# Kernel tuning notes

Hardware: AMD Instinct MI355X
Metric: run time of the kernel (lower is better)

## Reference

```python
import jax, jax.numpy as jnp
import numpy as np
from jax import lax

EPS = 1e-5
QUANT_BITS = 16  # Conv2dShift default input fixed-point bits


def round_fixed(x, quant_bits=QUANT_BITS):
    # fixed-point rounding of activations with straight-through estimator
    scale = 2.0 ** (quant_bits - 1)
    xq = jnp.round(x * scale) / scale
    return x + lax.stop_gradient(xq - x)


def shift_conv3x3(x, w_shift, stride=1):
    # w_shift already holds sign * 2^shift power-of-two weights (see setup)
    x = round_fixed(x)
    return lax.conv_general_dilated(
        x, w_shift, window_strides=(stride, stride), padding=[(1, 1), (1, 1)],
        dimension_numbers=("NCHW", "OIHW", "NCHW"))


def adder_conv3x3(x, w):
    # AdderNet: out[n,co,h,w] = -sum_{ci,kh,kw} |patch - w[co,ci,kh,kw]|
    Co = w.shape[0]
    # patches: [N, C*3*3, H, W], feature ordering (c, kh, kw) matches w.reshape
    p = lax.conv_general_dilated_patches(
        x, filter_shape=(3, 3), window_strides=(1, 1), padding=[(1, 1), (1, 1)])
    wf = w.reshape(Co, -1)

    def per_out_channel(wc):  # wc: [C*9]
        return -jnp.sum(jnp.abs(p - wc[None, :, None, None]), axis=1)  # [N,H,W]

    out = lax.map(per_out_channel, wf)  # [Co, N, H, W] (sequential: bounds memory)
    return jnp.transpose(out, (1, 0, 2, 3))


def batch_norm(x, gamma, beta):
    # training-mode BN (batch statistics), matching nn.BatchNorm2d default forward
    m = jnp.mean(x, axis=(0, 2, 3), keepdims=True)
    v = jnp.var(x, axis=(0, 2, 3), keepdims=True)
    xn = (x - m) * lax.rsqrt(v + EPS)
    return xn * gamma.reshape(1, -1, 1, 1) + beta.reshape(1, -1, 1, 1)


def _quantize_shift_weights(w, weight_bits=5):
    # DeepShift PS: weight -> sign * 2^round(log2|w|), shift clipped
    sign = jnp.where(w >= 0, 1.0, -1.0)
    shift = jnp.round(jnp.log2(jnp.abs(w) + 1e-12))
    shift = jnp.clip(shift, -(2.0 ** (weight_bits - 1) - 1.0), 0.0)
    return sign * jnp.exp2(shift)


def setup_inputs() -> dict:
    key = jax.random.key(0)
    ks = jax.random.split(key, 9)
    N, C, H, W = 64, 128, 32, 32
    planes = 128
    fan = 1.0 / np.sqrt(C * 9)
    x = jax.random.normal(ks[0], (N, C, H, W), dtype=jnp.float32)
    w_shift1 = _quantize_shift_weights(
        jax.random.normal(ks[1], (planes, C, 3, 3), dtype=jnp.float32) * fan)
    w_add1 = jax.random.normal(ks[2], (planes, planes, 3, 3), dtype=jnp.float32) * fan
    w_shift2 = _quantize_shift_weights(
        jax.random.normal(ks[3], (planes, planes, 3, 3), dtype=jnp.float32) * fan)
    w_add2 = jax.random.normal(ks[4], (planes, planes, 3, 3), dtype=jnp.float32) * fan
    gamma1 = jnp.ones((planes,), jnp.float32)
    beta1 = jnp.zeros((planes,), jnp.float32)
    gamma2 = jnp.ones((planes,), jnp.float32)
    beta2 = jnp.zeros((planes,), jnp.float32)
    return {"x": x, "w_shift1": w_shift1, "w_add1": w_add1, "gamma1": gamma1,
            "beta1": beta1, "w_shift2": w_shift2, "w_add2": w_add2,
            "gamma2": gamma2, "beta2": beta2}


def reference(x, w_shift1, w_add1, gamma1, beta1, w_shift2, w_add2, gamma2, beta2):
    residual = x
    out = shift_conv3x3(x, w_shift1, stride=1)
    out = adder_conv3x3(out, w_add1)
    out = jax.nn.relu(batch_norm(out, gamma1, beta1))
    out = shift_conv3x3(out, w_shift2, stride=1)
    out = adder_conv3x3(out, w_add2)
    out = batch_norm(out, gamma2, beta2)
    out = jax.nn.relu(out + residual)
    return out
```

## Files before the change

### kernel.cpp

```cpp
#include <hip/hip_runtime.h>


#define NB   64
#define CIN  128
#define HW   32
#define COUT 128
constexpr int PLANE    = HW * HW;
constexpr int NPAIR    = CIN / 2;
constexpr int CI_CHUNK = 4;
constexpr int CO_CHUNK = 8;
constexpr int LPLANE   = 34 * 32;
constexpr int LDS_TOT  = 2 * CI_CHUNK * LPLANE;
constexpr int A_CO     = 4;
constexpr int ASTRIDE  = 36;
constexpr float FSCALE    = 32768.0f;
constexpr float INV_SCALE = 1.0f / 32768.0f;
constexpr float QS     = 2048.0f;
constexpr float QB     = 32768.5f;
constexpr float INV_QS = 1.0f / 2048.0f;
constexpr unsigned PZ  = 0x80008000u;

constexpr int G_ROWB   = 32 * 4 * 16;
constexpr int G_CIQB   = 34 * G_ROWB;
constexpr int G_NB     = 4 * G_CIQB;

typedef _Float16 f16x8 __attribute__((ext_vector_type(8)));
typedef float    f32x4 __attribute__((ext_vector_type(4)));

#define GLOBAL_AS __attribute__((address_space(1)))
#define LDS_AS    __attribute__((address_space(3)))

__device__ __forceinline__ int fsw(int w) { return (w & 3) ^ ((w >> 2) & 3); }

__device__ __forceinline__ void gload_lds16(const void* g, void* l) {
    __builtin_amdgcn_global_load_lds((const GLOBAL_AS void*)g, (LDS_AS void*)l,
                                     16, 0, 0);
}
__device__ __forceinline__ float dpp_prev(float x) {
    return __int_as_float(__builtin_amdgcn_update_dpp(
        0, __float_as_int(x), 0x111, 0xF, 0xF, true));
}
__device__ __forceinline__ float dpp_next(float x) {
    return __int_as_float(__builtin_amdgcn_update_dpp(
        0, __float_as_int(x), 0x101, 0xF, 0xF, true));
}
__device__ __forceinline__ unsigned dpp_prev_u(unsigned x) {
    return (unsigned)__builtin_amdgcn_update_dpp(0, (int)x, 0x111, 0xF, 0xF, true);
}
__device__ __forceinline__ unsigned dpp_next_u(unsigned x) {
    return (unsigned)__builtin_amdgcn_update_dpp(0, (int)x, 0x101, 0xF, 0xF, true);
}
__device__ __forceinline__ uint4 dpp4_shr(uint4 v) {
    uint4 r;
    r.x = dpp_prev_u(v.x); r.y = dpp_prev_u(v.y);
    r.z = dpp_prev_u(v.z); r.w = dpp_prev_u(v.w);
    return r;
}
__device__ __forceinline__ uint4 dpp4_shl(uint4 v) {
    uint4 r;
    r.x = dpp_next_u(v.x); r.y = dpp_next_u(v.y);
    r.z = dpp_next_u(v.z); r.w = dpp_next_u(v.w);
    return r;
}
__device__ __forceinline__ void stage_plane4(const void* src, void* dst, int lane) {
#pragma unroll
    for (int i = 0; i < 4; ++i)
        gload_lds16((const char*)src + i * 1024 + lane * 16,
                    (char*)dst + 128 + i * 1024);
}
__device__ __forceinline__ unsigned q16(float a) {
    float t = fmaf(a, QS, QB);
    t = fminf(fmaxf(t, 0.0f), 65535.0f);
    return (unsigned)t;
}
__device__ __forceinline__ unsigned short f16b(float v) {
    return __builtin_bit_cast(unsigned short, (_Float16)v);
}

template <int WITH_BN>
__global__ __launch_bounds__(256) void transform_split(
    const float* __restrict__ in,
    const double* __restrict__ st, const float* __restrict__ gamma,
    const float* __restrict__ beta, uint4* __restrict__ G,
    const float* __restrict__ a1, const float* __restrict__ a2,
    const float* __restrict__ s1w, const float* __restrict__ s2w,
    unsigned* __restrict__ wqo, unsigned* __restrict__ WFd,
    double* __restrict__ stz)
{
    __shared__ float sT[32 * 132];
    __shared__ float sSC[32], sBI[32];
    const int tid = threadIdx.x;
    const int b   = blockIdx.x;

    if (!WITH_BN && b >= 2048) {
        if (b == 2048) { stz[tid] = 0.0; stz[tid + 256] = 0.0; }
        int i = (b - 2048) * 256 + tid;
        if (i < 147456) {
            int layer = i >= 73728;
            int j   = i - layer * 73728;
            int co  = j / 576;
            int rem = j - co * 576;
            int cp  = rem / 9;
            int tap = rem - cp * 9;
            const float* w = layer ? a2 : a1;
            float f0 = w[((size_t)co * CIN + 2 * cp) * 9 + tap];
            float f1 = w[((size_t)co * CIN + 2 * cp + 1) * 9 + tap];
            wqo[i] = q16(f0) | (q16(f1) << 16);
        } else {
            int j = i - 147456;
            int layer = j >= 73728;
            int idx = j - layer * 73728;
            int j2  = idx & 3;
            int l   = (idx >> 2) & 63;
            int cot = (idx >> 8) & 7;
            int ciq = (idx >> 11) & 3;
            int tap = idx >> 13;
            int ci  = ciq * 32 + (l >> 4) * 8 + j2 * 2;
            int co  = cot * 16 + (l & 15);
            const float* w = layer ? s2w : s1w;
            unsigned lo = f16b(w[((size_t)co * CIN + ci) * 9 + tap]);
            unsigned hi = f16b(w[((size_t)co * CIN + ci + 1) * 9 + tap]);
            WFd[layer * 73728 + idx] = lo | (hi << 16);
        }
        return;
    }

    const int n   = b >> 5;
    const int ciq = (b >> 3) & 3;
    const int rq  = b & 7;

    if (WITH_BN) {
        if (tid < 32) {
            int ch = ciq * 32 + tid;
            double m   = st[ch] / 65536.0;
            double var = st[128 + ch] / 65536.0 - m * m;
            double rstd = 1.0 / sqrt(var + 1e-5);
            float sc = (float)((double)gamma[ch] * rstd);
            sSC[tid] = sc;
            sBI[tid] = beta[ch] - (float)m * sc;
        }
        __syncthreads();
    }

#pragma unroll
    for (int it = 0; it < 4; ++it) {
        int flat = it * 256 + tid;
        int ci_rel = flat >> 5;
        int px4 = (flat & 31) * 4;
        const float* ap = in + ((size_t)(n * CIN + ciq * 32 + ci_rel)) * PLANE
                             + rq * 128 + px4;
        float4 v = *reinterpret_cast<const float4*>(ap);
        if (WITH_BN) {
            float sc = sSC[ci_rel], bs = sBI[ci_rel];
            v.x = fmaxf(fmaf(v.x, sc, bs), 0.0f);
            v.y = fmaxf(fmaf(v.y, sc, bs), 0.0f);
            v.z = fmaxf(fmaf(v.z, sc, bs), 0.0f);
            v.w = fmaxf(fmaf(v.w, sc, bs), 0.0f);
        }
        v.x = rintf(v.x * FSCALE) * INV_SCALE;
        v.y = rintf(v.y * FSCALE) * INV_SCALE;
        v.z = rintf(v.z * FSCALE) * INV_SCALE;
        v.w = rintf(v.w * FSCALE) * INV_SCALE;
        *reinterpret_cast<float4*>(&sT[ci_rel * 132 + px4]) = v;
    }
    __syncthreads();

    uint4* Gp = G + ((size_t)n * G_NB + ciq * G_CIQB) / 16;
#pragma unroll
    for (int it = 0; it < 2; ++it) {
        int f = it * 256 + tid;
        int row_loc = f >> 7;
        int rem = f & 127;
        int w  = rem >> 2;
        int sg = rem & 3;
        int g  = sg ^ fsw(w);
        uint4 u;
        unsigned* up = &u.x;
#pragma unroll
        for (int j2 = 0; j2 < 4; ++j2) {
            unsigned lo = f16b(sT[(g * 8 + 2 * j2)     * 132 + row_loc * 32 + w]);
            unsigned hi = f16b(sT[(g * 8 + 2 * j2 + 1) * 132 + row_loc * 32 + w]);
            up[j2] = lo | (hi << 16);
        }
        int gr = rq * 4 + row_loc + 1;
        Gp[(gr * 32 + w) * 4 + sg] = u;
    }
    if (rq == 0 && tid < 128) Gp[tid] = make_uint4(0, 0, 0, 0);
    if (rq == 7 && tid < 128) Gp[33 * 128 + tid] = make_uint4(0, 0, 0, 0);
}

__global__ __launch_bounds__(256, 2) void conv_mfma(
    const uint4* __restrict__ G, const uint4* __restrict__ WF,
    unsigned* __restrict__ P)
{
    __shared__ uint4 sA[3072];
    const int tid  = threadIdx.x;
    const int lane = tid & 63;
    const int wid  = tid >> 6;
    const int b    = (blockIdx.x & 7) * 64 + (blockIdx.x >> 3);
    const int n    = b >> 3;
    const int q4   = b & 7;
    const int gsg  = lane >> 4;

    char* myL = (char*)sA + wid * 12288;
    const char* src = (const char*)G + (size_t)n * G_NB + (size_t)q4 * 4 * G_ROWB
                    + wid * 2048;

    f32x4 acc[8][2];
#pragma unroll
    for (int i = 0; i < 8; ++i)
#pragma unroll
        for (int j = 0; j < 2; ++j) acc[i][j] = (f32x4){0.f, 0.f, 0.f, 0.f};

    auto stage = [&](int ciq, int buf) {
        const char* s = src + ciq * G_CIQB;
#pragma unroll
        for (int rr = 0; rr < 3; ++rr)
#pragma unroll
            for (int k = 0; k < 2; ++k)
                gload_lds16(s + rr * 2048 + k * 1024 + lane * 16,
                            myL + buf * 6144 + rr * 2048 + k * 1024);
    };

    stage(0, 0);
    for (int ciq = 0; ciq < 4; ++ciq) {
        const int buf = ciq & 1;
        if (ciq < 3) {
            stage(ciq + 1, buf ^ 1);
            asm volatile("s_waitcnt vmcnt(6)" ::: "memory");
        } else {
            asm volatile("s_waitcnt vmcnt(0)" ::: "memory");
        }
        __builtin_amdgcn_sched_barrier(0);

        uint4 Brow[2][3];
        int pwh[2];
#pragma unroll
        for (int half = 0; half < 2; ++half) {
            pwh[half] = half * 16 + (lane & 15);
#pragma unroll
            for (int rr = 0; rr < 3; ++rr)
                Brow[half][rr] = *reinterpret_cast<const uint4*>(
                    myL + buf * 6144 + rr * 2048 + pwh[half] * 64
                    + ((gsg ^ fsw(pwh[half])) * 16));
        }
#pragma unroll
        for (int dh = 0; dh < 3; ++dh)
#pragma unroll
        for (int dw = 0; dw < 3; ++dw) {
            const uint4* wfp = WF + ((size_t)((dh * 3 + dw) * 4 + ciq)) * 512 + lane;
            f16x8 a[8];
#pragma unroll
            for (int cot = 0; cot < 8; ++cot)
                a[cot] = __builtin_bit_cast(f16x8, wfp[cot * 64]);
#pragma unroll
            for (int half = 0; half < 2; ++half) {
                uint4 braw;
                if (dw == 1) {
                    braw = Brow[half][dh];
                } else if (dw == 0) {
                    if (half == 0) braw = dpp4_shr(Brow[0][dh]);
                    else {
                        int w2 = pwh[1] - 1;
                        braw = *reinterpret_cast<const uint4*>(
                            myL + buf * 6144 + dh * 2048 + w2 * 64
                            + ((gsg ^ fsw(w2)) * 16));
                    }
                } else {
                    if (half == 1) braw = dpp4_shl(Brow[1][dh]);
                    else {
                        int w2 = pwh[0] + 1;
                        braw = *reinterpret_cast<const uint4*>(
                            myL + buf * 6144 + dh * 2048 + w2 * 64
                            + ((gsg ^ fsw(w2)) * 16));
                    }
                }
                f16x8 bf = __builtin_bit_cast(f16x8, braw);
#pragma unroll
                for (int cot = 0; cot < 8; ++cot)
                    acc[cot][half] = __builtin_amdgcn_mfma_f32_16x16x32_f16(
                        a[cot], bf, acc[cot][half], 0, 0, 0);
            }
        }
    }

    unsigned* Pn = P + (size_t)n * NPAIR * PLANE;
    const int r = q4 * 4 + wid;
#pragma unroll
    for (int cot = 0; cot < 8; ++cot) {
        int cp = cot * 8 + (lane >> 4) * 2;
#pragma unroll
        for (int p = 0; p < 2; ++p) {
            int px = r * 32 + p * 16 + (lane & 15);
            unsigned u01 = q16(acc[cot][p][0]) | (q16(acc[cot][p][1]) << 16);
            unsigned u23 = q16(acc[cot][p][2]) | (q16(acc[cot][p][3]) << 16);
            Pn[cp * PLANE + px] = u01;
            Pn[(cp + 1) * PLANE + px] = u23;
        }
    }
}

__global__ __launch_bounds__(256, 2) void conv_shift_valu(
    const float* __restrict__ in, const float* __restrict__ wgt,
    unsigned* __restrict__ out)
{
    __shared__ __align__(16) float sIn[LDS_TOT];
    const int tid  = threadIdx.x;
    const int lane = tid & 63;
    const int wid  = tid >> 6;
    const int bid  = (blockIdx.x & 7) * 128 + (blockIdx.x >> 3);
    const int n    = bid >> 4;
    const int co0  = (bid & 15) * CO_CHUNK;
    const int r    = tid >> 3;
    const int c    = tid & 7;
    const int c0   = c * 4;
    const bool cz  = (c == 0), c7 = (c == 7);

    float acc[4][CO_CHUNK];
#pragma unroll
    for (int p = 0; p < 4; ++p)
#pragma unroll
        for (int co = 0; co < CO_CHUNK; ++co) acc[p][co] = 0.0f;

    const float* inN = in + (size_t)n * CIN * PLANE;
    for (int idx = tid; idx < 512; idx += 256) {
        int slot = idx >> 6, wq = idx & 63;
        sIn[slot * LPLANE + (wq < 32 ? wq : 1024 + wq)] = 0.0f;
    }
    stage_plane4(inN + wid * PLANE, sIn + wid * LPLANE, lane);
    __syncthreads();

    int cur = 0;
    for (int ci0 = 0; ci0 < CIN; ci0 += CI_CHUNK) {
        if (ci0 + CI_CHUNK < CIN)
            stage_plane4(inN + (size_t)(ci0 + CI_CHUNK + wid) * PLANE,
                         sIn + ((cur ^ 1) * CI_CHUNK + wid) * LPLANE, lane);
        const float* sb = sIn + cur * CI_CHUNK * LPLANE;
#pragma unroll
        for (int cc = 0; cc < CI_CHUNK; ++cc) {
            float w[3][6];
#pragma unroll
            for (int dh = 0; dh < 3; ++dh) {
                const float* sp = sb + cc * LPLANE + (r + dh) * 32 + c0;
                float4 qv = *reinterpret_cast<const float4*>(sp);
                qv.x = rintf(qv.x * FSCALE) * INV_SCALE;
                qv.y = rintf(qv.y * FSCALE) * INV_SCALE;
                qv.z = rintf(qv.z * FSCALE) * INV_SCALE;
                qv.w = rintf(qv.w * FSCALE) * INV_SCALE;
                float lf = dpp_prev(qv.w);
                float rt = dpp_next(qv.x);
                w[dh][0] = cz ? 0.0f : lf;
                w[dh][1] = qv.x; w[dh][2] = qv.y; w[dh][3] = qv.z; w[dh][4] = qv.w;
                w[dh][5] = c7 ? 0.0f : rt;
            }
            const float* wp = wgt + ((size_t)co0 * CIN + (ci0 + cc)) * 9;
#pragma unroll
            for (int co = 0; co < CO_CHUNK; ++co)
#pragma unroll
                for (int dh = 0; dh < 3; ++dh)
#pragma unroll
                    for (int dw = 0; dw < 3; ++dw) {
                        const float wvv = wp[(size_t)co * CIN * 9 + dh * 3 + dw];
#pragma unroll
                        for (int p = 0; p < 4; ++p)
                            acc[p][co] = fmaf(w[dh][p + dw], wvv, acc[p][co]);
                    }
        }
        __syncthreads();
        cur ^= 1;
    }
    unsigned* outP = out + ((size_t)n * NPAIR + co0 / 2) * PLANE + r * HW + c0;
#pragma unroll
    for (int pr = 0; pr < CO_CHUNK / 2; ++pr) {
        uint4 v;
        unsigned* vp = &v.x;
#pragma unroll
        for (int p = 0; p < 4; ++p)
            vp[p] = q16(acc[p][2 * pr]) | (q16(acc[p][2 * pr + 1]) << 16);
        *reinterpret_cast<uint4*>(&outP[pr * PLANE]) = v;
    }
}

__global__ __launch_bounds__(256) void bn_relu_inplace(
    float4* __restrict__ io, const float* __restrict__ scale,
    const float* __restrict__ bias)
{
    int i = blockIdx.x * 256 + threadIdx.x;
    int c = (i >> 8) & 127;
    float sc = scale[c], bs = bias[c];
    float4 v = io[i];
    v.x = fmaxf(fmaf(v.x, sc, bs), 0.0f);
    v.y = fmaxf(fmaf(v.y, sc, bs), 0.0f);
    v.z = fmaxf(fmaf(v.z, sc, bs), 0.0f);
    v.w = fmaxf(fmaf(v.w, sc, bs), 0.0f);
    io[i] = v;
}

__global__ __launch_bounds__(256, 8) void adder_packed(
    const unsigned* __restrict__ in, const unsigned* __restrict__ wq,
    float* __restrict__ out, double* __restrict__ ssum, double* __restrict__ ssq)
{
    __shared__ __align__(16) unsigned sRaw[4 + 133 * ASTRIDE];
    unsigned* sL = sRaw + 4;
    const int tid  = threadIdx.x;
    const int lane = tid & 63;
    const int bid  = (blockIdx.x & 7) * 256 + (blockIdx.x >> 3);
    const int n    = bid >> 5;
    const int co0  = (bid & 31) * A_CO;
    const int r    = tid >> 3;
    const int c0   = (tid & 7) * 4;
    const unsigned pz = PZ;

    for (int i = tid; i < 696; i += 256) {
        int addr;
        if (i < 4) {
            addr = i - 4;
        } else if (i < 184) {
            int j = i - 4;
            addr = (j / 36) * 33 * ASTRIDE + (j % 36);
        } else {
            int j = i - 184;
            int dr = j >> 2, col = 32 + (j & 3);
            int s = dr >> 5, rr = dr & 31;
            addr = (s * 33 + 1 + rr) * ASTRIDE + col;
        }
        sL[addr] = pz;
    }

    unsigned acc[4][A_CO];
#pragma unroll
    for (int p = 0; p < 4; ++p)
#pragma unroll
        for (int co = 0; co < A_CO; ++co) acc[p][co] = 0u;

    const uint4* inN4 = (const uint4*)(in + (size_t)n * NPAIR * PLANE);

    auto wslot = [&](int sl, uint4 v) {
        *reinterpret_cast<uint4*>(&sL[(sl * 33 + 1 + r) * ASTRIDE + c0]) = v;
    };

    uint4 rg0 = inN4[tid], rg1 = inN4[256 + tid];
    wslot(0, rg0); wslot(1, rg1);
    rg0 = inN4[512 + tid]; rg1 = inN4[768 + tid];
    __syncthreads();

    for (int s = 0; s < NPAIR / 2; ++s) {
        const int bsl = (s & 1) * 2;
#pragma unroll
        for (int cc = 0; cc < 2; ++cc) {
            unsigned wi[3][6];
#pragma unroll
            for (int dh = 0; dh < 3; ++dh) {
                const unsigned* rowp = &sL[((bsl + cc) * 33 + r + dh) * ASTRIDE];
                wi[dh][0] = rowp[c0 - 1];
                uint4 qv = *reinterpret_cast<const uint4*>(&rowp[c0]);
                wi[dh][1] = qv.x; wi[dh][2] = qv.y;
                wi[dh][3] = qv.z; wi[dh][4] = qv.w;
                wi[dh][5] = rowp[c0 + 4];
            }
            const int cp = 2 * s + cc;
            const unsigned* wrow = wq + ((size_t)co0 * NPAIR + cp) * 9;
#pragma unroll
            for (int co = 0; co < A_CO; ++co)
#pragma unroll
                for (int dh = 0; dh < 3; ++dh)
#pragma unroll
                    for (int dw = 0; dw < 3; ++dw) {
                        const unsigned wv =
                            wrow[(size_t)co * NPAIR * 9 + dh * 3 + dw];
#pragma unroll
                        for (int p = 0; p < 4; ++p)
                            asm("v_sad_u16 %0, %1, %2, %0"
                                : "+v"(acc[p][co])
                                : "v"(wi[dh][p + dw]), "s"(wv));
                    }
        }
        if (s + 1 < NPAIR / 2) {
            const int tsl = ((s + 1) & 1) * 2;
            wslot(tsl, rg0); wslot(tsl + 1, rg1);
        }
        if (s + 2 < NPAIR / 2) {
            rg0 = inN4[(2 * s + 4) * 256 + tid];
            rg1 = inN4[(2 * s + 5) * 256 + tid];
        }
        __syncthreads();
    }

    float* outP = out + ((size_t)n * COUT + co0) * PLANE + r * HW + c0;
#pragma unroll
    for (int co = 0; co < A_CO; ++co) {
        float y0 = -(float)acc[0][co] * INV_QS;
        float y1 = -(float)acc[1][co] * INV_QS;
        float y2 = -(float)acc[2][co] * INV_QS;
        float y3 = -(float)acc[3][co] * INV_QS;
        *reinterpret_cast<float4*>(&outP[co * PLANE]) = make_float4(y0, y1, y2, y3);
        float s = (y0 + y1) + (y2 + y3);
        float q = fmaf(y0, y0, y1 * y1) + fmaf(y2, y2, y3 * y3);
#pragma unroll
        for (int m = 32; m > 0; m >>= 1) {
            s += __shfl_xor(s, m, 64);
            q += __shfl_xor(q, m, 64);
        }
        if (lane == 0) {
            atomicAdd(&ssum[co0 + co], (double)s);
            atomicAdd(&ssq [co0 + co], (double)q);
        }
    }
}

__global__ __launch_bounds__(256) void prep_weights(
    const float* __restrict__ a1, const float* __restrict__ a2,
    unsigned* __restrict__ wqo, double* __restrict__ st)
{
    int i = blockIdx.x * 256 + threadIdx.x;
    if (blockIdx.x == 0) {
        st[threadIdx.x] = 0.0; st[threadIdx.x + 256] = 0.0;
    }
    int layer = i >= 73728;
    int j   = i - layer * 73728;
    int co  = j / 576;
    int rem = j - co * 576;
    int cp  = rem / 9;
    int tap = rem - cp * 9;
    const float* w = layer ? a2 : a1;
    float f0 = w[((size_t)co * CIN + 2 * cp) * 9 + tap];
    float f1 = w[((size_t)co * CIN + 2 * cp + 1) * 9 + tap];
    wqo[i] = q16(f0) | (q16(f1) << 16);
}

__global__ void finalize_bn(const double* __restrict__ ssum, const double* __restrict__ ssq,
                            const float* __restrict__ gamma, const float* __restrict__ beta,
                            float* __restrict__ scale, float* __restrict__ bias)
{
    int c = threadIdx.x;
    const double cnt = (double)NB * PLANE;
    double m   = ssum[c] / cnt;
    double var = ssq[c] / cnt - m * m;
    double rstd = 1.0 / sqrt(var + 1e-5);
    float sc = (float)((double)gamma[c] * rstd);
    scale[c] = sc;
    bias[c]  = beta[c] - (float)m * sc;
}

__global__ __launch_bounds__(256) void bn_add_relu(
    float4* __restrict__ io, const float4* __restrict__ res,
    const double* __restrict__ st, const float* __restrict__ gamma,
    const float* __restrict__ beta)
{
    int i = blockIdx.x * 256 + threadIdx.x;
    int c = (i >> 8) & 127;
    double m   = st[c] / 65536.0;
    double var = st[128 + c] / 65536.0 - m * m;
    double rstd = 1.0 / sqrt(var + 1e-5);
    float sc = (float)((double)gamma[c] * rstd);
    float bs = beta[c] - (float)m * sc;
    float4 v = io[i];
    float4 x = res[i];
    v.x = fmaxf(fmaf(v.x, sc, bs) + x.x, 0.0f);
    v.y = fmaxf(fmaf(v.y, sc, bs) + x.y, 0.0f);
    v.z = fmaxf(fmaf(v.z, sc, bs) + x.z, 0.0f);
    v.w = fmaxf(fmaf(v.w, sc, bs) + x.w, 0.0f);
    io[i] = v;
}

extern "C" void kernel_launch(void* const* d_in, const int* in_sizes, int n_in,
                              void* d_out, int out_size, void* d_ws, size_t ws_size,
                              hipStream_t stream)
{
    const float* x    = (const float*)d_in[0];
    const float* wS1  = (const float*)d_in[1];
    const float* wA1  = (const float*)d_in[2];
    const float* g1   = (const float*)d_in[3];
    const float* b1   = (const float*)d_in[4];
    const float* wS2  = (const float*)d_in[5];
    const float* wA2  = (const float*)d_in[6];
    const float* g2   = (const float*)d_in[7];
    const float* b2   = (const float*)d_in[8];
    float* outp = (float*)d_out;

    char* ws = (char*)d_ws;
    const size_t MFMA_WS = 35788800;
    const bool mf = ws_size >= MFMA_WS;

    unsigned* P = (unsigned*)ws;
    double* st; float* sb; unsigned* wq; char* Gb = nullptr; unsigned* WF = nullptr;
    if (mf) {
        Gb = ws + 16777216;
        st = (double*)(ws + 34603008);
        sb = (float*)(ws + 34607104);
        wq = (unsigned*)(ws + 34609152);
        WF = (unsigned*)(ws + 35198976);
    } else {
        st = (double*)(ws + 16777216);
        sb = (float*)(st + 512);
        wq = (unsigned*)(sb + 512);
    }
    double* s1 = st,       *q1 = st + 128;
    double* s2 = st + 256, *q2 = st + 384;
    float* sc1 = sb,       *bi1 = sb + 128;
    float* sc2 = sb + 256, *bi2 = sb + 384;

    const int adderGrid = NB * (COUT / A_CO);
    const int ewGrid    = (NB * COUT * PLANE / 4) / 256;

    if (mf) {
        transform_split<0><<<3200, 256, 0, stream>>>(
            x, nullptr, nullptr, nullptr, (uint4*)Gb,
            wA1, wA2, wS1, wS2, wq, WF, st);
        conv_mfma<<<512, 256, 0, stream>>>((const uint4*)Gb, (const uint4*)WF, P);
        adder_packed<<<adderGrid, 256, 0, stream>>>(P, wq, outp, s1, q1);
        transform_split<1><<<2048, 256, 0, stream>>>(
            outp, s1, g1, b1, (uint4*)Gb,
            nullptr, nullptr, nullptr, nullptr, nullptr, nullptr, nullptr);
        conv_mfma<<<512, 256, 0, stream>>>((const uint4*)Gb,
                                           (const uint4*)WF + 18432, P);
        adder_packed<<<adderGrid, 256, 0, stream>>>(P, wq + 73728, outp, s2, q2);
        bn_add_relu<<<ewGrid, 256, 0, stream>>>((float4*)outp, (const float4*)x,
                                                s2, g2, b2);
    } else {
        prep_weights<<<576, 256, 0, stream>>>(wA1, wA2, wq, st);
        conv_shift_valu<<<1024, 256, 0, stream>>>(x, wS1, P);
        adder_packed<<<adderGrid, 256, 0, stream>>>(P, wq, outp, s1, q1);
        finalize_bn<<<1, 128, 0, stream>>>(s1, q1, g1, b1, sc1, bi1);
        bn_relu_inplace<<<ewGrid, 256, 0, stream>>>((float4*)outp, sc1, bi1);
        conv_shift_valu<<<1024, 256, 0, stream>>>(outp, wS2, P);
        adder_packed<<<adderGrid, 256, 0, stream>>>(P, wq + 73728, outp, s2, q2);
        bn_add_relu<<<ewGrid, 256, 0, stream>>>((float4*)outp, (const float4*)x,
                                                s2, g2, b2);
    }
}
```

Measured before the change: 423.4 us.

## Drop padded LDS halo in adder kernel, use DPP neighbors and wave-staged planes

```diff
diff --git a/kernel.cpp b/kernel.cpp
--- a/kernel.cpp
+++ b/kernel.cpp
@@ -12,7 +12,6 @@
 constexpr int LPLANE   = 34 * 32;
 constexpr int LDS_TOT  = 2 * CI_CHUNK * LPLANE;
 constexpr int A_CO     = 4;
-constexpr int ASTRIDE  = 36;
 constexpr float FSCALE    = 32768.0f;
 constexpr float INV_SCALE = 1.0f / 32768.0f;
 constexpr float QS     = 2048.0f;
@@ -400,31 +399,22 @@
     const unsigned* __restrict__ in, const unsigned* __restrict__ wq,
     float* __restrict__ out, double* __restrict__ ssum, double* __restrict__ ssq)
 {
-    __shared__ __align__(16) unsigned sRaw[4 + 133 * ASTRIDE];
-    unsigned* sL = sRaw + 4;
+    __shared__ __align__(16) unsigned sIn[4 * LPLANE];
     const int tid  = threadIdx.x;
     const int lane = tid & 63;
+    const int wid  = tid >> 6;
     const int bid  = (blockIdx.x & 7) * 256 + (blockIdx.x >> 3);
     const int n    = bid >> 5;
     const int co0  = (bid & 31) * A_CO;
     const int r    = tid >> 3;
-    const int c0   = (tid & 7) * 4;
+    const int c    = tid & 7;
+    const int c0   = c * 4;
+    const bool cz  = (c == 0), c7 = (c == 7);
     const unsigned pz = PZ;
 
-    for (int i = tid; i < 696; i += 256) {
-        int addr;
-        if (i < 4) {
-            addr = i - 4;
-        } else if (i < 184) {
-            int j = i - 4;
-            addr = (j / 36) * 33 * ASTRIDE + (j % 36);
-        } else {
-            int j = i - 184;
-            int dr = j >> 2, col = 32 + (j & 3);
-            int s = dr >> 5, rr = dr & 31;
-            addr = (s * 33 + 1 + rr) * ASTRIDE + col;
-        }
-        sL[addr] = pz;
+    {
+        int slot = tid >> 6, wqi = tid & 63;
+        sIn[slot * LPLANE + (wqi < 32 ? wqi : 1024 + wqi)] = pz;
     }
 
     unsigned acc[4][A_CO];
@@ -433,30 +423,30 @@
 #pragma unroll
         for (int co = 0; co < A_CO; ++co) acc[p][co] = 0u;
 
-    const uint4* inN4 = (const uint4*)(in + (size_t)n * NPAIR * PLANE);
-
-    auto wslot = [&](int sl, uint4 v) {
-        *reinterpret_cast<uint4*>(&sL[(sl * 33 + 1 + r) * ASTRIDE + c0]) = v;
-    };
-
-    uint4 rg0 = inN4[tid], rg1 = inN4[256 + tid];
-    wslot(0, rg0); wslot(1, rg1);
-    rg0 = inN4[512 + tid]; rg1 = inN4[768 + tid];
+    const unsigned* inN = in + (size_t)n * NPAIR * PLANE;
+
+    stage_plane4(inN + (size_t)wid * PLANE, sIn + wid * LPLANE, lane);
     __syncthreads();
 
+    int cur = 0;
     for (int s = 0; s < NPAIR / 2; ++s) {
-        const int bsl = (s & 1) * 2;
+        if (s >= 1 && s + 1 < NPAIR / 2 && wid < 2)
+            stage_plane4(inN + (size_t)(2 * (s + 1) + wid) * PLANE,
+                         sIn + ((cur ^ 1) * 2 + wid) * LPLANE, lane);
+
+        const unsigned* sb = sIn + cur * 2 * LPLANE;
 #pragma unroll
         for (int cc = 0; cc < 2; ++cc) {
             unsigned wi[3][6];
 #pragma unroll
             for (int dh = 0; dh < 3; ++dh) {
-                const unsigned* rowp = &sL[((bsl + cc) * 33 + r + dh) * ASTRIDE];
-                wi[dh][0] = rowp[c0 - 1];
-                uint4 qv = *reinterpret_cast<const uint4*>(&rowp[c0]);
-                wi[dh][1] = qv.x; wi[dh][2] = qv.y;
-                wi[dh][3] = qv.z; wi[dh][4] = qv.w;
-                wi[dh][5] = rowp[c0 + 4];
+                const unsigned* sp = sb + cc * LPLANE + (r + dh) * 32 + c0;
+                uint4 qv = *reinterpret_cast<const uint4*>(sp);
+                unsigned lf = dpp_prev_u(qv.w);
+                unsigned rt = dpp_next_u(qv.x);
+                wi[dh][0] = cz ? pz : lf;
+                wi[dh][1] = qv.x; wi[dh][2] = qv.y; wi[dh][3] = qv.z; wi[dh][4] = qv.w;
+                wi[dh][5] = c7 ? pz : rt;
             }
             const int cp = 2 * s + cc;
             const unsigned* wrow = wq + ((size_t)co0 * NPAIR + cp) * 9;
@@ -475,15 +465,8 @@
                                 : "v"(wi[dh][p + dw]), "s"(wv));
                     }
         }
-        if (s + 1 < NPAIR / 2) {
-            const int tsl = ((s + 1) & 1) * 2;
-            wslot(tsl, rg0); wslot(tsl + 1, rg1);
-        }
-        if (s + 2 < NPAIR / 2) {
-            rg0 = inN4[(2 * s + 4) * 256 + tid];
-            rg1 = inN4[(2 * s + 5) * 256 + tid];
-        }
         __syncthreads();
+        cur ^= 1;
     }
 
     float* outP = out + ((size_t)n * COUT + co0) * PLANE + r * HW + c0;
```

New measurement: 412.4 us. 1.03x faster.
